# Kernel tuning notes

Hardware: AMD Instinct MI355X
Metric: run time of the kernel (lower is better)

The kernel has to match this reference:

```python
import jax, jax.numpy as jnp
from jax import lax
import numpy as np

B, T, F, H = 512, 256, 128, 256


def setup_inputs() -> dict:
    key = jax.random.key(0)
    ks = jax.random.split(key, 9)
    s = 0.05
    return {
        "X": jax.random.normal(ks[0], (B, T, F), dtype=jnp.float32),
        "attn1_W": jax.random.normal(ks[1], (T + 1, 2 * H + F), dtype=jnp.float32) * s,
        "attn1_b": jax.random.normal(ks[2], (T + 1,), dtype=jnp.float32) * s,
        "attn2_W": jax.random.normal(ks[3], (F, T + 1), dtype=jnp.float32) * s,
        "attn2_b": jax.random.normal(ks[4], (F,), dtype=jnp.float32) * s,
        "W_ih": jax.random.normal(ks[5], (4 * H, F), dtype=jnp.float32) * s,
        "W_hh": jax.random.normal(ks[6], (4 * H, H), dtype=jnp.float32) * s,
        "b_ih": jax.random.normal(ks[7], (4 * H,), dtype=jnp.float32) * s,
        "b_hh": jax.random.normal(ks[8], (4 * H,), dtype=jnp.float32) * s,
    }


def reference(X, attn1_W, attn1_b, attn2_W, attn2_b, W_ih, W_hh, b_ih, b_hh):
    b, t, f = X.shape
    h_dim = W_hh.shape[1]

    def step(carry, x_t):
        h, c = carry
        # input attention: concat [x, h, c] -> tanh(linear) -> linear -> gate x
        z = jnp.concatenate([x_t, h, c], axis=1)  # [B, F+2H]
        a = jnp.tanh(z @ attn1_W.T + attn1_b)      # [B, T+1]
        xi = (a @ attn2_W.T + attn2_b) * x_t       # [B, F]
        # LSTMCell (PyTorch gate order: i, f, g, o)
        gates = xi @ W_ih.T + b_ih + h @ W_hh.T + b_hh  # [B, 4H]
        i_g, f_g, g_g, o_g = jnp.split(gates, 4, axis=1)
        i_g = jax.nn.sigmoid(i_g)
        f_g = jax.nn.sigmoid(f_g)
        g_g = jnp.tanh(g_g)
        o_g = jax.nn.sigmoid(o_g)
        c_new = f_g * c + i_g * g_g
        h_new = o_g * jnp.tanh(c_new)
        return (h_new, c_new), (h_new, c_new)

    h0 = jnp.zeros((b, h_dim), dtype=X.dtype)
    c0 = jnp.zeros((b, h_dim), dtype=X.dtype)
    _, (hs, cs) = lax.scan(step, (h0, c0), jnp.swapaxes(X, 0, 1))  # [T,B,H]
    return jnp.swapaxes(hs, 0, 1), jnp.swapaxes(cs, 0, 1)  # [B,T,H]
```

## Files before the change

### kernel.cpp

```cpp
#include <hip/hip_runtime.h>


#define Bb 512
#define Tt 256
#define Ff 128
#define Hh 256

typedef unsigned short ushort_t;
typedef short s16x8 __attribute__((ext_vector_type(8)));
typedef float f32x4 __attribute__((ext_vector_type(4)));

#define A1_NT 17
#define A1_NK 20
#define A2_NT 8
#define A2_NK 9
#define IH_NT 64
#define IH_NK 4
#define HH_NT 64
#define HH_NK 8
#define CH_A1 0
#define CH_A2 21760
#define CH_IH 26368
#define CH_HH 42752
#define CH_TOTAL 75520

#define ZP 648
#define AP 296
#define XIP 136
#define XP 132
#define GP 1028

__device__ inline ushort_t f2b(float f) {
    unsigned u = __float_as_uint(f);
    unsigned r = (u + 0x7fffu + ((u >> 16) & 1u)) >> 16;
    return (ushort_t)r;
}
__device__ inline float fast_sig(float x) { return 1.f / (1.f + __expf(-x)); }
__device__ inline float fast_tanh(float x) {
    float cx = fminf(fmaxf(x, -15.f), 15.f);
    float e = __expf(2.f * cx);
    return (e - 1.f) / (e + 1.f);
}

__global__ void conv_kernel(const float* __restrict__ a1,
                            const float* __restrict__ a2,
                            const float* __restrict__ ih,
                            const float* __restrict__ hh,
                            ushort_t* __restrict__ ws) {
    int idx = blockIdx.x * 256 + threadIdx.x;
    if (idx >= CH_TOTAL) return;
    int lane = idx & 63;
    int jo = lane & 15;
    int ko = (lane >> 4) * 8;
    float v[8];
    if (idx < CH_A2) {
        int cix = idx >> 6;
        int tile = cix / A1_NK, kc = cix % A1_NK;
        int j = tile * 16 + jo, k = kc * 32 + ko;
        #pragma unroll
        for (int e = 0; e < 8; ++e) v[e] = (j < 257) ? a1[j * 640 + k + e] : 0.f;
    } else if (idx < CH_IH) {
        int cix = (idx - CH_A2) >> 6;
        int tile = cix / A2_NK, kc = cix % A2_NK;
        int j = tile * 16 + jo, k = kc * 32 + ko;
        #pragma unroll
        for (int e = 0; e < 8; ++e) v[e] = (k + e < 257) ? a2[j * 257 + k + e] : 0.f;
    } else if (idx < CH_HH) {
        int cix = (idx - CH_IH) >> 6;
        int tile = cix / IH_NK, kc = cix % IH_NK;
        int j = tile * 16 + jo, k = kc * 32 + ko;
        #pragma unroll
        for (int e = 0; e < 8; ++e) v[e] = ih[j * 128 + k + e];
    } else {
        int cix = (idx - CH_HH) >> 6;
        int tile = cix / HH_NK, kc = cix % HH_NK;
        int j = tile * 16 + jo, k = kc * 32 + ko;
        #pragma unroll
        for (int e = 0; e < 8; ++e) v[e] = hh[j * 256 + k + e];
    }
    union { s16x8 v8; ushort_t u[8]; } o;
    #pragma unroll
    for (int e = 0; e < 8; ++e) o.u[e] = f2b(v[e]);
    ((s16x8*)ws)[idx] = o.v8;
}

__global__ __launch_bounds__(1024) void lstm_mfma(
    const float* __restrict__ X,
    const float* __restrict__ b1,
    const float* __restrict__ b2,
    const float* __restrict__ bih,
    const float* __restrict__ bhh,
    const ushort_t* __restrict__ wsw,
    float* __restrict__ out)
{
    __shared__ ushort_t z_bf[16][ZP];
    __shared__ ushort_t a_bf[16][AP];
    __shared__ ushort_t xi_bf[16][XIP];
    __shared__ float    s_x[16][XP];
    __shared__ float    s_g[16][GP];
    __shared__ float    s_c[16][256];

    const int tid = threadIdx.x;
    const int w   = tid >> 6;
    const int l   = tid & 63;
    const int lj  = l & 15;
    const int lr4 = (l >> 4) * 4;
    const int lk8 = (l >> 4) * 8;
    const int b0  = blockIdx.x * 16;

    const s16x8* __restrict__ W8 = (const s16x8*)wsw;

    float b1v0 = 0.f, b1v1 = 0.f;
    { int j = w * 16 + lj; if (j < 257) b1v0 = b1[j]; }
    if (w == 0) { int j = 256 + lj; if (j < 257) b1v1 = b1[j]; }
    float b2v = 0.f;
    if (w >= 8) b2v = b2[(w - 8) * 16 + lj];
    float bg[4];
    #pragma unroll
    for (int i = 0; i < 4; ++i) { int j = (4 * w + i) * 16 + lj; bg[i] = bih[j] + bhh[j]; }

    for (int i = tid; i < 16 * 512; i += 1024) {
        int r = i >> 9, k = i & 511;
        z_bf[r][128 + k] = 0;
    }
    for (int i = tid; i < 16 * AP; i += 1024) {
        int r = i / AP, k = i - r * AP;
        a_bf[r][k] = 0;
    }
    for (int i = tid; i < 16 * 256; i += 1024) {
        int r = i >> 8, d = i & 255;
        s_c[r][d] = 0.f;
    }
    if (tid < 512) {
        int r = tid >> 5, c4 = (tid & 31) * 4;
        float4 xv = *(const float4*)&X[((size_t)(b0 + r) * Tt + 0) * Ff + c4];
        s_x[r][c4] = xv.x; s_x[r][c4 + 1] = xv.y; s_x[r][c4 + 2] = xv.z; s_x[r][c4 + 3] = xv.w;
        z_bf[r][c4] = f2b(xv.x); z_bf[r][c4 + 1] = f2b(xv.y);
        z_bf[r][c4 + 2] = f2b(xv.z); z_bf[r][c4 + 3] = f2b(xv.w);
    }
    __syncthreads();

    float* __restrict__ hs = out;
    float* __restrict__ cs = out + (size_t)Bb * Tt * Hh;

    f32x4 agate[4];

    for (int t = 0; t < Tt; ++t) {
        {
            f32x4 acc = {0.f, 0.f, 0.f, 0.f};
            const s16x8* wp = W8 + CH_A1 + (w * A1_NK) * 64 + l;
            #pragma unroll 4
            for (int kc = 0; kc < A1_NK; ++kc) {
                s16x8 a = *(const s16x8*)&z_bf[lj][kc * 32 + lk8];
                acc = __builtin_amdgcn_mfma_f32_16x16x32_bf16(a, wp[kc * 64], acc, 0, 0, 0);
            }
            int j = w * 16 + lj;
            if (j < 257) {
                #pragma unroll
                for (int q = 0; q < 4; ++q)
                    a_bf[lr4 + q][j] = f2b(fast_tanh(acc[q] + b1v0));
            }
        }
        if (w == 0) {
            f32x4 acc = {0.f, 0.f, 0.f, 0.f};
            const s16x8* wp = W8 + CH_A1 + (16 * A1_NK) * 64 + l;
            #pragma unroll 4
            for (int kc = 0; kc < A1_NK; ++kc) {
                s16x8 a = *(const s16x8*)&z_bf[lj][kc * 32 + lk8];
                acc = __builtin_amdgcn_mfma_f32_16x16x32_bf16(a, wp[kc * 64], acc, 0, 0, 0);
            }
            int j = 256 + lj;
            if (j < 257) {
                #pragma unroll
                for (int q = 0; q < 4; ++q)
                    a_bf[lr4 + q][j] = f2b(fast_tanh(acc[q] + b1v1));
            }
        }
        {
            s16x8 ah[HH_NK];
            #pragma unroll
            for (int kc = 0; kc < HH_NK; ++kc)
                ah[kc] = *(const s16x8*)&z_bf[lj][128 + kc * 32 + lk8];
            #pragma unroll
            for (int i = 0; i < 4; ++i) {
                f32x4 acc = {0.f, 0.f, 0.f, 0.f};
                const s16x8* wp = W8 + CH_HH + ((4 * w + i) * HH_NK) * 64 + l;
                #pragma unroll
                for (int kc = 0; kc < HH_NK; ++kc)
                    acc = __builtin_amdgcn_mfma_f32_16x16x32_bf16(ah[kc], wp[kc * 64], acc, 0, 0, 0);
                agate[i] = acc;
            }
        }
        __syncthreads();

        if (w >= 8) {
            int p = w - 8;
            f32x4 acc = {0.f, 0.f, 0.f, 0.f};
            const s16x8* wp = W8 + CH_A2 + (p * A2_NK) * 64 + l;
            #pragma unroll 3
            for (int kc = 0; kc < A2_NK; ++kc) {
                s16x8 a = *(const s16x8*)&a_bf[lj][kc * 32 + lk8];
                acc = __builtin_amdgcn_mfma_f32_16x16x32_bf16(a, wp[kc * 64], acc, 0, 0, 0);
            }
            int j = p * 16 + lj;
            #pragma unroll
            for (int q = 0; q < 4; ++q) {
                int r = lr4 + q;
                float xi = (acc[q] + b2v) * s_x[r][j];
                xi_bf[r][j] = f2b(xi);
            }
        }
        __syncthreads();

        {
            s16x8 ax[IH_NK];
            #pragma unroll
            for (int kc = 0; kc < IH_NK; ++kc)
                ax[kc] = *(const s16x8*)&xi_bf[lj][kc * 32 + lk8];
            #pragma unroll
            for (int i = 0; i < 4; ++i) {
                f32x4 acc = agate[i];
                const s16x8* wp = W8 + CH_IH + ((4 * w + i) * IH_NK) * 64 + l;
                #pragma unroll
                for (int kc = 0; kc < IH_NK; ++kc)
                    acc = __builtin_amdgcn_mfma_f32_16x16x32_bf16(ax[kc], wp[kc * 64], acc, 0, 0, 0);
                int j = (4 * w + i) * 16 + lj;
                #pragma unroll
                for (int q = 0; q < 4; ++q)
                    s_g[lr4 + q][j] = acc[q] + bg[i];
            }
        }
        __syncthreads();

        float4 xv;
        int xr = 0, xc = 0;
        bool ldx = (t + 1 < Tt) && (tid < 512);
        if (ldx) {
            xr = tid >> 5; xc = (tid & 31) * 4;
            xv = *(const float4*)&X[((size_t)(b0 + xr) * Tt + (t + 1)) * Ff + xc];
        }
        #pragma unroll
        for (int p4 = 0; p4 < 4; ++p4) {
            int r = p4 * 4 + (tid >> 8);
            int d = tid & 255;
            float gi = s_g[r][d];
            float gf = s_g[r][d + 256];
            float gg = s_g[r][d + 512];
            float go = s_g[r][d + 768];
            float ig = fast_sig(gi);
            float fg = fast_sig(gf);
            float g_g = fast_tanh(gg);
            float og = fast_sig(go);
            float cn = fmaf(fg, s_c[r][d], ig * g_g);
            float hn = og * fast_tanh(cn);
            s_c[r][d] = cn;
            z_bf[r][128 + d] = f2b(hn);
            z_bf[r][384 + d] = f2b(cn);
            size_t oi = ((size_t)(b0 + r) * Tt + t) * Hh + d;
            hs[oi] = hn;
            cs[oi] = cn;
        }
        if (ldx) {
            s_x[xr][xc] = xv.x; s_x[xr][xc + 1] = xv.y; s_x[xr][xc + 2] = xv.z; s_x[xr][xc + 3] = xv.w;
            z_bf[xr][xc] = f2b(xv.x); z_bf[xr][xc + 1] = f2b(xv.y);
            z_bf[xr][xc + 2] = f2b(xv.z); z_bf[xr][xc + 3] = f2b(xv.w);
        }
        __syncthreads();
    }
}

extern "C" void kernel_launch(void* const* d_in, const int* in_sizes, int n_in,
                              void* d_out, int out_size, void* d_ws, size_t ws_size,
                              hipStream_t stream) {
    const float* X   = (const float*)d_in[0];
    const float* a1W = (const float*)d_in[1];
    const float* a1b = (const float*)d_in[2];
    const float* a2W = (const float*)d_in[3];
    const float* a2b = (const float*)d_in[4];
    const float* Wih = (const float*)d_in[5];
    const float* Whh = (const float*)d_in[6];
    const float* bih = (const float*)d_in[7];
    const float* bhh = (const float*)d_in[8];
    ushort_t* ws = (ushort_t*)d_ws;

    hipLaunchKernelGGL(conv_kernel, dim3(CH_TOTAL / 256), dim3(256), 0, stream,
                       a1W, a2W, Wih, Whh, ws);
    hipLaunchKernelGGL(lstm_mfma, dim3(32), dim3(1024), 0, stream,
                       X, a1b, a2b, bih, bhh, ws, (float*)d_out);
}
```

Baseline: 6.474 ms.

## Keep all weights resident in registers with warp-specialized roles and register-held LSTM state

Each wave now preloads its slice of the bf16 weights into a 96-entry register array once, instead of re-reading them from global memory every timestep. Waves are given fixed roles: waves 0-3 do the attention-1 GEMM (wave 4 also covers the extra output column), waves 4-7 do attention-2, and waves 8-15 do the gate GEMMs. The gate waves apply the LSTM cell directly from their MFMA accumulators and keep c in registers, which removes the s_g/s_c/s_x shared buffers and one barrier per step. The cost is very high register pressure, which risks spills and caps occupancy. The x gating now multiplies by the bf16-rounded x instead of fp32 x, a small precision change.

```diff
diff --git a/kernel.cpp b/kernel.cpp
--- a/kernel.cpp
+++ b/kernel.cpp
@@ -10,13 +10,9 @@
 typedef short s16x8 __attribute__((ext_vector_type(8)));
 typedef float f32x4 __attribute__((ext_vector_type(4)));
 
-#define A1_NT 17
 #define A1_NK 20
-#define A2_NT 8
 #define A2_NK 9
-#define IH_NT 64
 #define IH_NK 4
-#define HH_NT 64
 #define HH_NK 8
 #define CH_A1 0
 #define CH_A2 21760
@@ -27,13 +23,14 @@
 #define ZP 648
 #define AP 296
 #define XIP 136
-#define XP 132
-#define GP 1028
 
 __device__ inline ushort_t f2b(float f) {
     unsigned u = __float_as_uint(f);
     unsigned r = (u + 0x7fffu + ((u >> 16) & 1u)) >> 16;
     return (ushort_t)r;
+}
+__device__ inline float b2f(ushort_t u) {
+    return __uint_as_float(((unsigned)u) << 16);
 }
 __device__ inline float fast_sig(float x) { return 1.f / (1.f + __expf(-x)); }
 __device__ inline float fast_tanh(float x) {
@@ -96,9 +93,6 @@
     __shared__ ushort_t z_bf[16][ZP];
     __shared__ ushort_t a_bf[16][AP];
     __shared__ ushort_t xi_bf[16][XIP];
-    __shared__ float    s_x[16][XP];
-    __shared__ float    s_g[16][GP];
-    __shared__ float    s_c[16][256];
 
     const int tid = threadIdx.x;
     const int w   = tid >> 6;
@@ -110,160 +104,210 @@
 
     const s16x8* __restrict__ W8 = (const s16x8*)wsw;
 
-    float b1v0 = 0.f, b1v1 = 0.f;
-    { int j = w * 16 + lj; if (j < 257) b1v0 = b1[j]; }
-    if (w == 0) { int j = 256 + lj; if (j < 257) b1v1 = b1[j]; }
-    float b2v = 0.f;
-    if (w >= 8) b2v = b2[(w - 8) * 16 + lj];
-    float bg[4];
+    s16x8 wreg[96];
+    float bA1[4] = {0.f, 0.f, 0.f, 0.f};
+    float b1_256 = 0.f;
+    float bA2[2] = {0.f, 0.f};
+    float bgq[8];
     #pragma unroll
-    for (int i = 0; i < 4; ++i) { int j = (4 * w + i) * 16 + lj; bg[i] = bih[j] + bhh[j]; }
-
-    for (int i = tid; i < 16 * 512; i += 1024) {
-        int r = i >> 9, k = i & 511;
-        z_bf[r][128 + k] = 0;
-    }
-    for (int i = tid; i < 16 * AP; i += 1024) {
-        int r = i / AP, k = i - r * AP;
-        a_bf[r][k] = 0;
-    }
-    for (int i = tid; i < 16 * 256; i += 1024) {
-        int r = i >> 8, d = i & 255;
-        s_c[r][d] = 0.f;
-    }
-    if (tid < 512) {
-        int r = tid >> 5, c4 = (tid & 31) * 4;
-        float4 xv = *(const float4*)&X[((size_t)(b0 + r) * Tt + 0) * Ff + c4];
-        s_x[r][c4] = xv.x; s_x[r][c4 + 1] = xv.y; s_x[r][c4 + 2] = xv.z; s_x[r][c4 + 3] = xv.w;
-        z_bf[r][c4] = f2b(xv.x); z_bf[r][c4 + 1] = f2b(xv.y);
-        z_bf[r][c4 + 2] = f2b(xv.z); z_bf[r][c4 + 3] = f2b(xv.w);
+    for (int u = 0; u < 8; ++u) bgq[u] = 0.f;
+
+    if (w < 4) {
+        #pragma unroll
+        for (int t2 = 0; t2 < 4; ++t2) {
+            #pragma unroll
+            for (int kc = 0; kc < A1_NK; ++kc)
+                wreg[t2 * A1_NK + kc] = W8[CH_A1 + ((4 * w + t2) * A1_NK + kc) * 64 + l];
+            bA1[t2] = b1[64 * w + 16 * t2 + lj];
+        }
+    } else if (w < 8) {
+        int p = w - 4;
+        #pragma unroll
+        for (int t2 = 0; t2 < 2; ++t2) {
+            #pragma unroll
+            for (int kc = 0; kc < A2_NK; ++kc)
+                wreg[t2 * A2_NK + kc] = W8[CH_A2 + ((2 * p + t2) * A2_NK + kc) * 64 + l];
+            bA2[t2] = b2[32 * p + 16 * t2 + lj];
+        }
+        if (w == 4) {
+            #pragma unroll
+            for (int kc = 0; kc < A1_NK; ++kc)
+                wreg[18 + kc] = W8[CH_A1 + (16 * A1_NK + kc) * 64 + l];
+            b1_256 = b1[256];
+        }
+    } else {
+        int g = w - 8;
+        #pragma unroll
+        for (int q = 0; q < 2; ++q) {
+            #pragma unroll
+            for (int i = 0; i < 4; ++i) {
+                int n = i * 16 + q * 8 + g;
+                int u = q * 4 + i;
+                #pragma unroll
+                for (int kc = 0; kc < HH_NK; ++kc)
+                    wreg[u * 8 + kc] = W8[CH_HH + (n * HH_NK + kc) * 64 + l];
+                #pragma unroll
+                for (int kc = 0; kc < IH_NK; ++kc)
+                    wreg[64 + u * 4 + kc] = W8[CH_IH + (n * IH_NK + kc) * 64 + l];
+                int j = 256 * i + 128 * q + 16 * g + lj;
+                bgq[u] = bih[j] + bhh[j];
+            }
+        }
+    }
+
+    f32x4 agate[8];
+    float c_reg[8];
+    #pragma unroll
+    for (int u = 0; u < 8; ++u) c_reg[u] = 0.f;
+
+    {
+        int i = tid;
+        int r = i >> 6, c = (i & 63) * 8;
+        s16x8 zz = {0, 0, 0, 0, 0, 0, 0, 0};
+        *(s16x8*)&z_bf[r][128 + c] = zz;
+    }
+    if (tid < 592) {
+        int r = tid / 37, c = (tid - r * 37) * 8;
+        s16x8 zz = {0, 0, 0, 0, 0, 0, 0, 0};
+        *(s16x8*)&a_bf[r][c] = zz;
+    }
+    if (tid < 256) {
+        int r = tid >> 4, c = (tid & 15) * 8;
+        float4 x0 = *(const float4*)&X[((size_t)(b0 + r) * Tt) * Ff + c];
+        float4 x1 = *(const float4*)&X[((size_t)(b0 + r) * Tt) * Ff + c + 4];
+        s16x8 v;
+        v[0] = (short)f2b(x0.x); v[1] = (short)f2b(x0.y);
+        v[2] = (short)f2b(x0.z); v[3] = (short)f2b(x0.w);
+        v[4] = (short)f2b(x1.x); v[5] = (short)f2b(x1.y);
+        v[6] = (short)f2b(x1.z); v[7] = (short)f2b(x1.w);
+        *(s16x8*)&z_bf[r][c] = v;
     }
     __syncthreads();
 
     float* __restrict__ hs = out;
     float* __restrict__ cs = out + (size_t)Bb * Tt * Hh;
 
-    f32x4 agate[4];
+    float4 xp0, xp1;
 
     for (int t = 0; t < Tt; ++t) {
-        {
-            f32x4 acc = {0.f, 0.f, 0.f, 0.f};
-            const s16x8* wp = W8 + CH_A1 + (w * A1_NK) * 64 + l;
-            #pragma unroll 4
+        if (w < 4) {
+            f32x4 acc[4];
+            #pragma unroll
+            for (int t2 = 0; t2 < 4; ++t2) acc[t2] = (f32x4){0.f, 0.f, 0.f, 0.f};
+            #pragma unroll
             for (int kc = 0; kc < A1_NK; ++kc) {
                 s16x8 a = *(const s16x8*)&z_bf[lj][kc * 32 + lk8];
-                acc = __builtin_amdgcn_mfma_f32_16x16x32_bf16(a, wp[kc * 64], acc, 0, 0, 0);
-            }
-            int j = w * 16 + lj;
-            if (j < 257) {
+                #pragma unroll
+                for (int t2 = 0; t2 < 4; ++t2)
+                    acc[t2] = __builtin_amdgcn_mfma_f32_16x16x32_bf16(a, wreg[t2 * A1_NK + kc], acc[t2], 0, 0, 0);
+            }
+            #pragma unroll
+            for (int t2 = 0; t2 < 4; ++t2) {
+                int j = 64 * w + 16 * t2 + lj;
                 #pragma unroll
                 for (int q = 0; q < 4; ++q)
-                    a_bf[lr4 + q][j] = f2b(fast_tanh(acc[q] + b1v0));
-            }
-        }
-        if (w == 0) {
+                    a_bf[lr4 + q][j] = f2b(fast_tanh(acc[t2][q] + bA1[t2]));
+            }
+        } else if (w == 4) {
             f32x4 acc = {0.f, 0.f, 0.f, 0.f};
-            const s16x8* wp = W8 + CH_A1 + (16 * A1_NK) * 64 + l;
-            #pragma unroll 4
+            #pragma unroll
             for (int kc = 0; kc < A1_NK; ++kc) {
                 s16x8 a = *(const s16x8*)&z_bf[lj][kc * 32 + lk8];
-                acc = __builtin_amdgcn_mfma_f32_16x16x32_bf16(a, wp[kc * 64], acc, 0, 0, 0);
-            }
-            int j = 256 + lj;
-            if (j < 257) {
+                acc = __builtin_amdgcn_mfma_f32_16x16x32_bf16(a, wreg[18 + kc], acc, 0, 0, 0);
+            }
+            if (lj == 0) {
                 #pragma unroll
                 for (int q = 0; q < 4; ++q)
-                    a_bf[lr4 + q][j] = f2b(fast_tanh(acc[q] + b1v1));
-            }
-        }
-        {
-            s16x8 ah[HH_NK];
-            #pragma unroll
-            for (int kc = 0; kc < HH_NK; ++kc)
-                ah[kc] = *(const s16x8*)&z_bf[lj][128 + kc * 32 + lk8];
-            #pragma unroll
-            for (int i = 0; i < 4; ++i) {
-                f32x4 acc = {0.f, 0.f, 0.f, 0.f};
-                const s16x8* wp = W8 + CH_HH + ((4 * w + i) * HH_NK) * 64 + l;
-                #pragma unroll
-                for (int kc = 0; kc < HH_NK; ++kc)
-                    acc = __builtin_amdgcn_mfma_f32_16x16x32_bf16(ah[kc], wp[kc * 64], acc, 0, 0, 0);
-                agate[i] = acc;
+                    a_bf[lr4 + q][256] = f2b(fast_tanh(acc[q] + b1_256));
+            }
+        } else if (w >= 8) {
+            #pragma unroll
+            for (int u = 0; u < 8; ++u)
+                agate[u] = (f32x4){bgq[u], bgq[u], bgq[u], bgq[u]};
+            #pragma unroll
+            for (int kc = 0; kc < HH_NK; ++kc) {
+                s16x8 a = *(const s16x8*)&z_bf[lj][128 + kc * 32 + lk8];
+                #pragma unroll
+                for (int u = 0; u < 8; ++u)
+                    agate[u] = __builtin_amdgcn_mfma_f32_16x16x32_bf16(a, wreg[u * 8 + kc], agate[u], 0, 0, 0);
             }
         }
         __syncthreads();
 
-        if (w >= 8) {
-            int p = w - 8;
-            f32x4 acc = {0.f, 0.f, 0.f, 0.f};
-            const s16x8* wp = W8 + CH_A2 + (p * A2_NK) * 64 + l;
-            #pragma unroll 3
+        if (w < 4) {
+            if (t + 1 < Tt) {
+                const float* xs = &X[((size_t)(b0 + (tid >> 4)) * Tt + (t + 1)) * Ff + (tid & 15) * 8];
+                xp0 = *(const float4*)xs;
+                xp1 = *(const float4*)(xs + 4);
+            }
+        } else if (w < 8) {
+            f32x4 acc[2];
+            acc[0] = (f32x4){0.f, 0.f, 0.f, 0.f};
+            acc[1] = (f32x4){0.f, 0.f, 0.f, 0.f};
+            #pragma unroll
             for (int kc = 0; kc < A2_NK; ++kc) {
                 s16x8 a = *(const s16x8*)&a_bf[lj][kc * 32 + lk8];
-                acc = __builtin_amdgcn_mfma_f32_16x16x32_bf16(a, wp[kc * 64], acc, 0, 0, 0);
-            }
-            int j = p * 16 + lj;
-            #pragma unroll
-            for (int q = 0; q < 4; ++q) {
-                int r = lr4 + q;
-                float xi = (acc[q] + b2v) * s_x[r][j];
-                xi_bf[r][j] = f2b(xi);
+                #pragma unroll
+                for (int t2 = 0; t2 < 2; ++t2)
+                    acc[t2] = __builtin_amdgcn_mfma_f32_16x16x32_bf16(a, wreg[t2 * A2_NK + kc], acc[t2], 0, 0, 0);
+            }
+            #pragma unroll
+            for (int t2 = 0; t2 < 2; ++t2) {
+                int j = 32 * (w - 4) + 16 * t2 + lj;
+                #pragma unroll
+                for (int q = 0; q < 4; ++q) {
+                    int r = lr4 + q;
+                    float xf = b2f(z_bf[r][j]);
+                    float xi = (acc[t2][q] + bA2[t2]) * xf;
+                    xi_bf[r][j] = f2b(xi);
+                }
             }
         }
         __syncthreads();
 
-        {
-            s16x8 ax[IH_NK];
-            #pragma unroll
-            for (int kc = 0; kc < IH_NK; ++kc)
-                ax[kc] = *(const s16x8*)&xi_bf[lj][kc * 32 + lk8];
-            #pragma unroll
-            for (int i = 0; i < 4; ++i) {
-                f32x4 acc = agate[i];
-                const s16x8* wp = W8 + CH_IH + ((4 * w + i) * IH_NK) * 64 + l;
-                #pragma unroll
-                for (int kc = 0; kc < IH_NK; ++kc)
-                    acc = __builtin_amdgcn_mfma_f32_16x16x32_bf16(ax[kc], wp[kc * 64], acc, 0, 0, 0);
-                int j = (4 * w + i) * 16 + lj;
-                #pragma unroll
-                for (int q = 0; q < 4; ++q)
-                    s_g[lr4 + q][j] = acc[q] + bg[i];
-            }
-        }
-        __syncthreads();
-
-        float4 xv;
-        int xr = 0, xc = 0;
-        bool ldx = (t + 1 < Tt) && (tid < 512);
-        if (ldx) {
-            xr = tid >> 5; xc = (tid & 31) * 4;
-            xv = *(const float4*)&X[((size_t)(b0 + xr) * Tt + (t + 1)) * Ff + xc];
-        }
-        #pragma unroll
-        for (int p4 = 0; p4 < 4; ++p4) {
-            int r = p4 * 4 + (tid >> 8);
-            int d = tid & 255;
-            float gi = s_g[r][d];
-            float gf = s_g[r][d + 256];
-            float gg = s_g[r][d + 512];
-            float go = s_g[r][d + 768];
-            float ig = fast_sig(gi);
-            float fg = fast_sig(gf);
-            float g_g = fast_tanh(gg);
-            float og = fast_sig(go);
-            float cn = fmaf(fg, s_c[r][d], ig * g_g);
-            float hn = og * fast_tanh(cn);
-            s_c[r][d] = cn;
-            z_bf[r][128 + d] = f2b(hn);
-            z_bf[r][384 + d] = f2b(cn);
-            size_t oi = ((size_t)(b0 + r) * Tt + t) * Hh + d;
-            hs[oi] = hn;
-            cs[oi] = cn;
-        }
-        if (ldx) {
-            s_x[xr][xc] = xv.x; s_x[xr][xc + 1] = xv.y; s_x[xr][xc + 2] = xv.z; s_x[xr][xc + 3] = xv.w;
-            z_bf[xr][xc] = f2b(xv.x); z_bf[xr][xc + 1] = f2b(xv.y);
-            z_bf[xr][xc + 2] = f2b(xv.z); z_bf[xr][xc + 3] = f2b(xv.w);
+        if (w >= 8) {
+            #pragma unroll
+            for (int kc = 0; kc < IH_NK; ++kc) {
+                s16x8 a = *(const s16x8*)&xi_bf[lj][kc * 32 + lk8];
+                #pragma unroll
+                for (int u = 0; u < 8; ++u)
+                    agate[u] = __builtin_amdgcn_mfma_f32_16x16x32_bf16(a, wreg[64 + u * 4 + kc], agate[u], 0, 0, 0);
+            }
+            int g = w - 8;
+            #pragma unroll
+            for (int q = 0; q < 2; ++q) {
+                int d = 128 * q + 16 * g + lj;
+                #pragma unroll
+                for (int qq = 0; qq < 4; ++qq) {
+                    int r = lr4 + qq;
+                    float gi = agate[q * 4 + 0][qq];
+                    float gf = agate[q * 4 + 1][qq];
+                    float gg = agate[q * 4 + 2][qq];
+                    float go = agate[q * 4 + 3][qq];
+                    float ig = fast_sig(gi);
+                    float fg = fast_sig(gf);
+                    float g_g = fast_tanh(gg);
+                    float og = fast_sig(go);
+                    float cn = fmaf(fg, c_reg[q * 4 + qq], ig * g_g);
+                    float hn = og * fast_tanh(cn);
+                    c_reg[q * 4 + qq] = cn;
+                    z_bf[r][128 + d] = f2b(hn);
+                    z_bf[r][384 + d] = f2b(cn);
+                    size_t oi = ((size_t)(b0 + r) * Tt + t) * Hh + d;
+                    hs[oi] = hn;
+                    cs[oi] = cn;
+                }
+            }
+        } else if (w < 4) {
+            if (t + 1 < Tt) {
+                int r = tid >> 4, c = (tid & 15) * 8;
+                s16x8 v;
+                v[0] = (short)f2b(xp0.x); v[1] = (short)f2b(xp0.y);
+                v[2] = (short)f2b(xp0.z); v[3] = (short)f2b(xp0.w);
+                v[4] = (short)f2b(xp1.x); v[5] = (short)f2b(xp1.y);
+                v[6] = (short)f2b(xp1.z); v[7] = (short)f2b(xp1.w);
+                *(s16x8*)&z_bf[r][c] = v;
+            }
         }
         __syncthreads();
     }
```

After: 10.63 ms. 64.2% more time.
